# Performance work log

Measured on AMD Instinct MI355X. Metric: run time of the kernel, lower is better.

## Reference

```python
import jax, jax.numpy as jnp
from jax import lax
import numpy as np

H = 512      # hidden_size
NF = 64      # nfeatures
NL = 2       # num_layers
OUT = 1      # output_size
B, T = 64, 512


def _uniform(key, shape, scale):
    return jax.random.uniform(key, shape, jnp.float32, -scale, scale)


def setup_inputs() -> dict:
    key = jax.random.key(0)
    ks = jax.random.split(key, 12)
    s = 1.0 / np.sqrt(H)  # PyTorch LSTM/Linear init scale
    return {
        "x": jax.random.normal(ks[0], (B, T, NF), jnp.float32),
        # layer 0 (input NF -> H), PyTorch gate order i,f,g,o along 4H axis
        "W_ih0": _uniform(ks[1], (4 * H, NF), s),
        "W_hh0": _uniform(ks[2], (4 * H, H), s),
        "b_ih0": _uniform(ks[3], (4 * H,), s),
        "b_hh0": _uniform(ks[4], (4 * H,), s),
        # layer 1 (input H -> H)
        "W_ih1": _uniform(ks[5], (4 * H, H), s),
        "W_hh1": _uniform(ks[6], (4 * H, H), s),
        "b_ih1": _uniform(ks[7], (4 * H,), s),
        "b_hh1": _uniform(ks[8], (4 * H,), s),
        # final linear head
        "W_fc": _uniform(ks[9], (OUT, H), s),
        "b_fc": _uniform(ks[10], (OUT,), s),
    }


def _lstm_layer(x, W_ih, W_hh, b_ih, b_hh):
    """x: [B, T, D_in] -> hidden sequence [B, T, H]. Zero initial state."""
    b, t, _ = x.shape
    h0 = jnp.zeros((b, H), x.dtype)
    c0 = jnp.zeros((b, H), x.dtype)
    # precompute input projections for all timesteps: [T, B, 4H]
    xp = jnp.swapaxes(jnp.einsum('btd,gd->btg', x, W_ih) + b_ih + b_hh, 0, 1)

    def step(carry, xt):
        h, c = carry
        gates = xt + h @ W_hh.T  # [B, 4H]
        i, f, g, o = jnp.split(gates, 4, axis=-1)
        i = jax.nn.sigmoid(i)
        f = jax.nn.sigmoid(f)
        g = jnp.tanh(g)
        o = jax.nn.sigmoid(o)
        c = f * c + i * g
        h = o * jnp.tanh(c)
        return (h, c), h

    _, hs = lax.scan(step, (h0, c0), xp)  # hs: [T, B, H]
    return jnp.swapaxes(hs, 0, 1)


def reference(x, W_ih0, W_hh0, b_ih0, b_hh0, W_ih1, W_hh1, b_ih1, b_hh1, W_fc, b_fc):
    h = _lstm_layer(x, W_ih0, W_hh0, b_ih0, b_hh0)
    h = _lstm_layer(h, W_ih1, W_hh1, b_ih1, b_hh1)
    return h @ W_fc.T + b_fc  # [B, T, OUT]
```

## Files before the change

### kernel.cpp

```cpp
#include <hip/hip_runtime.h>

#define T_STEPS 512
#define BATCH   64
#define HID     512
#define NSLICE  32

typedef __attribute__((ext_vector_type(8))) short short8;
typedef __attribute__((ext_vector_type(4))) float f32x4;

__device__ __forceinline__ unsigned short f2bf(float f){
  unsigned u = __float_as_uint(f);
  u += 0x7FFF + ((u >> 16) & 1);
  return (unsigned short)(u >> 16);
}
__device__ __forceinline__ float bf2f(unsigned short s){
  return __uint_as_float(((unsigned)s) << 16);
}
__device__ __forceinline__ f32x4 mfma16(short8 a, short8 b, f32x4 c){
  return __builtin_amdgcn_mfma_f32_16x16x32_bf16(a, b, c, 0, 0, 0);
}
__device__ __forceinline__ float sigf(float x){
  return 1.0f / (1.0f + exp2f(-1.44269504f * x));
}
__device__ __forceinline__ float tanh_(float x){
  float e = exp2f(2.88539008f * x);
  return 1.0f - 2.0f / (1.0f + e);
}

__device__ __forceinline__ void waitGE(int* p, int target){
  int guard = 0;
  while (__hip_atomic_load(p, __ATOMIC_RELAXED, __HIP_MEMORY_SCOPE_AGENT) < target){
    __builtin_amdgcn_s_sleep(1);
    if (++guard > (1 << 22)) break;
  }
  asm volatile("" ::: "memory");
  __builtin_amdgcn_fence(__ATOMIC_ACQUIRE, "workgroup");
}

__device__ __forceinline__ void signal(int* p){
  __builtin_amdgcn_fence(__ATOMIC_RELEASE, "workgroup");
  asm volatile("" ::: "memory");
  __hip_atomic_fetch_add(p, 1, __ATOMIC_RELAXED, __HIP_MEMORY_SCOPE_AGENT);
}

template<int NKB>
__device__ __forceinline__ void loadB(const unsigned short* __restrict__ Wg, int K, int kstart,
                                      int l15, int l4, short8 B[4][NKB]){
  #pragma unroll
  for (int tt = 0; tt < 4; ++tt)
    #pragma unroll
    for (int kb = 0; kb < NKB; ++kb)
      B[tt][kb] = *(const short8*)(Wg + (long)(tt*16 + l15)*K + kstart + kb*32 + l4*8);
}

template<int NKB>
__device__ __forceinline__ void gemmA(const unsigned short* __restrict__ Ab, long rs,
                                      int l15, int l4, const short8 B[4][NKB], f32x4 acc[4][4]){
  #pragma unroll
  for (int kb = 0; kb < NKB; ++kb){
    short8 a[4];
    #pragma unroll
    for (int m = 0; m < 4; ++m)
      a[m] = *(const short8*)(Ab + (long)(m*16 + l15)*rs + kb*32 + l4*8);
    #pragma unroll
    for (int m = 0; m < 4; ++m)
      #pragma unroll
      for (int tt = 0; tt < 4; ++tt)
        acc[m][tt] = mfma16(B[tt][kb], a[m], acc[m][tt]);
  }
}

__device__ __forceinline__ void reduceWrite(float* red, int w, int l15, int l4, f32x4 acc[4][4]){
  #pragma unroll
  for (int m = 0; m < 4; ++m){
    if (m == w) continue;
    int mi = (m > w) ? m - 1 : m;
    #pragma unroll
    for (int tt = 0; tt < 4; ++tt){
      float* p = red + (w*12 + mi*4 + tt)*320 + l15*20 + l4*4;
      *(f32x4*)p = acc[m][tt];
    }
  }
}
__device__ __forceinline__ void reduceRead(const float* red, int w, int l15, int l4,
                                           f32x4 gf[4], f32x4 acc[4][4]){
  #pragma unroll
  for (int tt = 0; tt < 4; ++tt) gf[tt] = acc[w][tt];
  #pragma unroll
  for (int v = 0; v < 4; ++v){
    if (v == w) continue;
    int mi = (w > v) ? w - 1 : w;
    #pragma unroll
    for (int tt = 0; tt < 4; ++tt){
      const float* p = red + (v*12 + mi*4 + tt)*320 + l15*20 + l4*4;
      gf[tt] += *(const f32x4*)p;
    }
  }
}

__device__ __forceinline__ void gatesStore(f32x4 gf[4], f32x4& cst,
                                           unsigned short* __restrict__ hdst){
  f32x4 hh;
  #pragma unroll
  for (int r = 0; r < 4; ++r){
    float iv = sigf(gf[0][r]), fv = sigf(gf[1][r]);
    float gv = tanh_(gf[2][r]), ov = sigf(gf[3][r]);
    float cv = fv * cst[r] + iv * gv;
    cst[r] = cv;
    hh[r] = ov * tanh_(cv);
  }
  unsigned long long pk = (unsigned long long)f2bf(hh[0])
    | ((unsigned long long)f2bf(hh[1]) << 16)
    | ((unsigned long long)f2bf(hh[2]) << 32)
    | ((unsigned long long)f2bf(hh[3]) << 48);
  __hip_atomic_store((unsigned long long*)hdst, pk, __ATOMIC_RELAXED, __HIP_MEMORY_SCOPE_AGENT);
}

template<int NXB, int NHB>
__device__ void l0_loop(int g, int w, int lane,
                        const unsigned short* __restrict__ Wg,
                        const float* __restrict__ bias0,
                        const unsigned short* __restrict__ xb,
                        unsigned short* __restrict__ h0seq,
                        int* cnt0, float* red, int hk0){
  int l15 = lane & 15, l4 = lane >> 4;
  short8 Bx[4][(NXB > 0) ? NXB : 1];
  if constexpr (NXB > 0) loadB<NXB>(Wg, 576, 0, l15, l4, Bx);
  short8 Bh[4][NHB];
  loadB<NHB>(Wg, 576, 64 + hk0, l15, l4, Bh);
  f32x4 bsv[4];
  #pragma unroll
  for (int tt = 0; tt < 4; ++tt) bsv[tt] = *(const f32x4*)&bias0[(g*4 + tt)*16 + l4*4];
  f32x4 cst = {0.f, 0.f, 0.f, 0.f};
  int b = w*16 + l15, colb = g*16 + l4*4;

  for (int t = 0; t < T_STEPS; ++t){
    if (t) waitGE(&cnt0[t-1], NSLICE);
    f32x4 acc[4][4];
    #pragma unroll
    for (int m = 0; m < 4; ++m)
      #pragma unroll
      for (int tt = 0; tt < 4; ++tt) acc[m][tt] = (f32x4){0.f,0.f,0.f,0.f};
    if constexpr (NXB > 0)
      gemmA<NXB>(xb + (long)t*64, (long)T_STEPS*64, l15, l4, Bx, acc);
    if (t)
      gemmA<NHB>(h0seq + (long)(t-1)*BATCH*HID + hk0, HID, l15, l4, Bh, acc);
    reduceWrite(red, w, l15, l4, acc);
    __syncthreads();
    f32x4 gf[4];
    reduceRead(red, w, l15, l4, gf, acc);
    #pragma unroll
    for (int tt = 0; tt < 4; ++tt) gf[tt] += bsv[tt];
    gatesStore(gf, cst, h0seq + (long)t*BATCH*HID + (long)b*HID + colb);
    __syncthreads();
    if (threadIdx.x == 0) signal(&cnt0[t]);
  }
}

__device__ void l1_loop(int g, int w, int lane,
                        const unsigned short* __restrict__ Wg,
                        const float* __restrict__ bias1,
                        const unsigned short* __restrict__ h0seq,
                        unsigned short* __restrict__ h1seq,
                        int* cnt0, int* cnt1, float* red){
  int l15 = lane & 15, l4 = lane >> 4;
  short8 Bh[4][8];
  loadB<8>(Wg, 1024, w*256, l15, l4, Bh);
  f32x4 bsv[4];
  #pragma unroll
  for (int tt = 0; tt < 4; ++tt) bsv[tt] = *(const f32x4*)&bias1[(g*4 + tt)*16 + l4*4];
  f32x4 cst = {0.f, 0.f, 0.f, 0.f};
  int b = w*16 + l15, colb = g*16 + l4*4;

  for (int t = 0; t < T_STEPS; ++t){
    waitGE(&cnt0[t], NSLICE);
    if (t) waitGE(&cnt1[t-1], NSLICE);
    f32x4 acc[4][4];
    #pragma unroll
    for (int m = 0; m < 4; ++m)
      #pragma unroll
      for (int tt = 0; tt < 4; ++tt) acc[m][tt] = (f32x4){0.f,0.f,0.f,0.f};
    if (w < 2)
      gemmA<8>(h0seq + (long)t*BATCH*HID + w*256, HID, l15, l4, Bh, acc);
    else if (t)
      gemmA<8>(h1seq + (long)(t-1)*BATCH*HID + (w-2)*256, HID, l15, l4, Bh, acc);
    reduceWrite(red, w, l15, l4, acc);
    __syncthreads();
    f32x4 gf[4];
    reduceRead(red, w, l15, l4, gf, acc);
    #pragma unroll
    for (int tt = 0; tt < 4; ++tt) gf[tt] += bsv[tt];
    gatesStore(gf, cst, h1seq + (long)t*BATCH*HID + (long)b*HID + colb);
    __syncthreads();
    if (threadIdx.x == 0) signal(&cnt1[t]);
  }
}

extern "C" __global__ void __launch_bounds__(256, 1)
lstm_persist(const unsigned short* __restrict__ Wpk0,
             const unsigned short* __restrict__ Wpk1,
             const float* __restrict__ bias0, const float* __restrict__ bias1,
             const unsigned short* __restrict__ xb,
             unsigned short* __restrict__ h0seq, unsigned short* __restrict__ h1seq,
             int* cnt0, int* cnt1){
  __shared__ float red[15360];
  int wg = blockIdx.x;
  int role = wg >> 5;
  int g = wg & 31;
  int w = threadIdx.x >> 6;
  int lane = threadIdx.x & 63;

  if (role == 0){
    const unsigned short* Wg = Wpk0 + (long)g*4*16*576;
    switch (w){
      case 0:  l0_loop<2,3>(g, 0, lane, Wg, bias0, xb, h0seq, cnt0, red, 0);   break;
      case 1:  l0_loop<0,5>(g, 1, lane, Wg, bias0, xb, h0seq, cnt0, red, 96);  break;
      case 2:  l0_loop<0,4>(g, 2, lane, Wg, bias0, xb, h0seq, cnt0, red, 256); break;
      default: l0_loop<0,4>(g, 3, lane, Wg, bias0, xb, h0seq, cnt0, red, 384); break;
    }
  } else {
    const unsigned short* Wg = Wpk1 + (long)g*4*16*1024;
    l1_loop(g, w, lane, Wg, bias1, h0seq, h1seq, cnt0, cnt1, red);
  }
}

extern "C" __global__ void prep_kernel(const float* __restrict__ x,
    const float* __restrict__ Wih0, const float* __restrict__ Whh0,
    const float* __restrict__ bih0, const float* __restrict__ bhh0,
    const float* __restrict__ Wih1, const float* __restrict__ Whh1,
    const float* __restrict__ bih1, const float* __restrict__ bhh1,
    unsigned short* __restrict__ Wpk0, unsigned short* __restrict__ Wpk1,
    float* __restrict__ bias0, float* __restrict__ bias1,
    unsigned short* __restrict__ xb, int* __restrict__ syncm){
  long gid = (long)blockIdx.x * blockDim.x + threadIdx.x;
  long gs  = (long)gridDim.x * blockDim.x;
  const long NW0 = 32L*4*16*576;
  const long NW1 = 32L*4*16*1024;
  const long NX  = 64L*512*64;

  for (long i = gid; i < NW0; i += gs){
    int k = (int)(i % 576);
    long q = i / 576;
    int r  = (int)(q & 15);
    long q2 = q >> 4;
    int tt = (int)(q2 & 3);
    int g  = (int)(q2 >> 2);
    int row = tt*512 + g*16 + r;
    float v = (k < 64) ? Wih0[(long)row*64 + k] : Whh0[(long)row*512 + (k - 64)];
    Wpk0[i] = f2bf(v);
  }
  for (long i = gid; i < NW1; i += gs){
    int k = (int)(i & 1023);
    long q = i >> 10;
    int r  = (int)(q & 15);
    long q2 = q >> 4;
    int tt = (int)(q2 & 3);
    int g  = (int)(q2 >> 2);
    int row = tt*512 + g*16 + r;
    float v = (k < 512) ? Wih1[(long)row*512 + k] : Whh1[(long)row*512 + (k - 512)];
    Wpk1[i] = f2bf(v);
  }
  for (long i = gid; i < 2048; i += gs){
    int r = (int)(i & 15);
    int tt = (int)((i >> 4) & 3);
    int g  = (int)(i >> 6);
    int row = tt*512 + g*16 + r;
    bias0[i] = bih0[row] + bhh0[row];
    bias1[i] = bih1[row] + bhh1[row];
  }
  for (long i = gid; i < NX; i += gs) xb[i] = f2bf(x[i]);
  for (long i = gid; i < 1024; i += gs) syncm[i] = 0;
}

extern "C" __global__ void head_kernel(const unsigned short* __restrict__ h1seq,
    const float* __restrict__ wfc, const float* __restrict__ bfc,
    float* __restrict__ out){
  int t = blockIdx.x;
  int tid = threadIdx.x;
  int b = tid >> 2, q = tid & 3;
  const unsigned short* hp = h1seq + ((long)t*BATCH + b)*HID + q*128;
  const float* wp = wfc + q*128;
  float s = 0.f;
  #pragma unroll
  for (int i = 0; i < 16; ++i){
    short8 v = *(const short8*)(hp + i*8);
    #pragma unroll
    for (int e = 0; e < 8; ++e)
      s += bf2f((unsigned short)v[e]) * wp[i*8 + e];
  }
  s += __shfl_xor(s, 1, 64);
  s += __shfl_xor(s, 2, 64);
  if (q == 0) out[(long)b*T_STEPS + t] = s + bfc[0];
}

extern "C" void kernel_launch(void* const* d_in, const int* in_sizes, int n_in,
                              void* d_out, int out_size, void* d_ws, size_t ws_size,
                              hipStream_t stream){
  const float* x    = (const float*)d_in[0];
  const float* Wih0 = (const float*)d_in[1];
  const float* Whh0 = (const float*)d_in[2];
  const float* bih0 = (const float*)d_in[3];
  const float* bhh0 = (const float*)d_in[4];
  const float* Wih1 = (const float*)d_in[5];
  const float* Whh1 = (const float*)d_in[6];
  const float* bih1 = (const float*)d_in[7];
  const float* bhh1 = (const float*)d_in[8];
  const float* wfc  = (const float*)d_in[9];
  const float* bfc  = (const float*)d_in[10];
  float* out = (float*)d_out;

  char* p = (char*)d_ws;
  auto carve = [&](size_t bytes) -> void* {
    void* r = (void*)p;
    p += (bytes + 255) & ~(size_t)255;
    return r;
  };
  unsigned short* Wpk0  = (unsigned short*)carve(32L*4*16*576*2);
  unsigned short* Wpk1  = (unsigned short*)carve(32L*4*16*1024*2);
  float* bias0 = (float*)carve(2048*4);
  float* bias1 = (float*)carve(2048*4);
  unsigned short* xb    = (unsigned short*)carve(64L*512*64*2);
  unsigned short* h0seq = (unsigned short*)carve(512L*64*512*2);
  unsigned short* h1seq = (unsigned short*)carve(512L*64*512*2);
  int* syncm   = (int*)carve(4096);
  int* cnt0 = syncm;
  int* cnt1 = syncm + 512;

  hipLaunchKernelGGL(prep_kernel, dim3(1024), dim3(256), 0, stream,
                     x, Wih0, Whh0, bih0, bhh0, Wih1, Whh1, bih1, bhh1,
                     Wpk0, Wpk1, bias0, bias1, xb, syncm);
  hipLaunchKernelGGL(lstm_persist, dim3(64), dim3(256), 0, stream,
                     Wpk0, Wpk1, bias0, bias1, xb, h0seq, h1seq, cnt0, cnt1);
  hipLaunchKernelGGL(head_kernel, dim3(512), dim3(256), 0, stream,
                     h1seq, wfc, bfc, out);
}
```

Measured before the change: 5.249 ms.

## Replace atomic counter barriers with per-block padded flag slots polled by one wave

```diff
diff --git a/kernel.cpp b/kernel.cpp
--- a/kernel.cpp
+++ b/kernel.cpp
@@ -3,7 +3,6 @@
 #define T_STEPS 512
 #define BATCH   64
 #define HID     512
-#define NSLICE  32
 
 typedef __attribute__((ext_vector_type(8))) short short8;
 typedef __attribute__((ext_vector_type(4))) float f32x4;
@@ -27,20 +26,47 @@
   return 1.0f - 2.0f / (1.0f + e);
 }
 
-__device__ __forceinline__ void waitGE(int* p, int target){
-  int guard = 0;
-  while (__hip_atomic_load(p, __ATOMIC_RELAXED, __HIP_MEMORY_SCOPE_AGENT) < target){
-    __builtin_amdgcn_s_sleep(1);
-    if (++guard > (1 << 22)) break;
-  }
+
+__device__ __forceinline__ void pollL0(const int* flags0, int target){
+  if (threadIdx.x < 64){
+    int lane = threadIdx.x;
+    int guard = 0;
+    for (;;){
+      int v = (lane < 32)
+        ? __hip_atomic_load(&flags0[lane*32], __ATOMIC_RELAXED, __HIP_MEMORY_SCOPE_AGENT)
+        : target;
+      if (__ballot(v >= target) == ~0ull) break;
+      __builtin_amdgcn_s_sleep(1);
+      if (++guard > (1 << 20)) break;
+    }
+  }
+  __builtin_amdgcn_fence(__ATOMIC_ACQUIRE, "workgroup");
   asm volatile("" ::: "memory");
+  __syncthreads();
+}
+
+__device__ __forceinline__ void pollL1(const int* flags0, const int* flags1, int t){
+  if (threadIdx.x < 64){
+    int lane = threadIdx.x;
+    const int* p = (lane < 32) ? &flags0[lane*32] : &flags1[(lane-32)*32];
+    int tgt = (lane < 32) ? t + 1 : t;
+    int guard = 0;
+    for (;;){
+      int v = __hip_atomic_load(p, __ATOMIC_RELAXED, __HIP_MEMORY_SCOPE_AGENT);
+      if (__ballot(v >= tgt) == ~0ull) break;
+      __builtin_amdgcn_s_sleep(1);
+      if (++guard > (1 << 20)) break;
+    }
+  }
   __builtin_amdgcn_fence(__ATOMIC_ACQUIRE, "workgroup");
-}
-
-__device__ __forceinline__ void signal(int* p){
+  asm volatile("" ::: "memory");
+  __syncthreads();
+}
+
+__device__ __forceinline__ void signalSlot(int* slot, int val){
   __builtin_amdgcn_fence(__ATOMIC_RELEASE, "workgroup");
   asm volatile("" ::: "memory");
-  __hip_atomic_fetch_add(p, 1, __ATOMIC_RELAXED, __HIP_MEMORY_SCOPE_AGENT);
+  __hip_atomic_store(slot, val, __ATOMIC_RELAXED, __HIP_MEMORY_SCOPE_AGENT);
 }
 
 template<int NKB>
@@ -122,7 +148,7 @@
                         const float* __restrict__ bias0,
                         const unsigned short* __restrict__ xb,
                         unsigned short* __restrict__ h0seq,
-                        int* cnt0, float* red, int hk0){
+                        int* flags0, float* red, int hk0){
   int l15 = lane & 15, l4 = lane >> 4;
   short8 Bx[4][(NXB > 0) ? NXB : 1];
   if constexpr (NXB > 0) loadB<NXB>(Wg, 576, 0, l15, l4, Bx);
@@ -135,7 +161,6 @@
   int b = w*16 + l15, colb = g*16 + l4*4;
 
   for (int t = 0; t < T_STEPS; ++t){
-    if (t) waitGE(&cnt0[t-1], NSLICE);
     f32x4 acc[4][4];
     #pragma unroll
     for (int m = 0; m < 4; ++m)
@@ -143,6 +168,7 @@
       for (int tt = 0; tt < 4; ++tt) acc[m][tt] = (f32x4){0.f,0.f,0.f,0.f};
     if constexpr (NXB > 0)
       gemmA<NXB>(xb + (long)t*64, (long)T_STEPS*64, l15, l4, Bx, acc);
+    if (t) pollL0(flags0, t);
     if (t)
       gemmA<NHB>(h0seq + (long)(t-1)*BATCH*HID + hk0, HID, l15, l4, Bh, acc);
     reduceWrite(red, w, l15, l4, acc);
@@ -153,7 +179,7 @@
     for (int tt = 0; tt < 4; ++tt) gf[tt] += bsv[tt];
     gatesStore(gf, cst, h0seq + (long)t*BATCH*HID + (long)b*HID + colb);
     __syncthreads();
-    if (threadIdx.x == 0) signal(&cnt0[t]);
+    if (threadIdx.x == 0) signalSlot(&flags0[g*32], t + 1);
   }
 }
 
@@ -162,7 +188,7 @@
                         const float* __restrict__ bias1,
                         const unsigned short* __restrict__ h0seq,
                         unsigned short* __restrict__ h1seq,
-                        int* cnt0, int* cnt1, float* red){
+                        int* flags0, int* flags1, float* red){
   int l15 = lane & 15, l4 = lane >> 4;
   short8 Bh[4][8];
   loadB<8>(Wg, 1024, w*256, l15, l4, Bh);
@@ -173,8 +199,7 @@
   int b = w*16 + l15, colb = g*16 + l4*4;
 
   for (int t = 0; t < T_STEPS; ++t){
-    waitGE(&cnt0[t], NSLICE);
-    if (t) waitGE(&cnt1[t-1], NSLICE);
+    pollL1(flags0, flags1, t);
     f32x4 acc[4][4];
     #pragma unroll
     for (int m = 0; m < 4; ++m)
@@ -192,7 +217,7 @@
     for (int tt = 0; tt < 4; ++tt) gf[tt] += bsv[tt];
     gatesStore(gf, cst, h1seq + (long)t*BATCH*HID + (long)b*HID + colb);
     __syncthreads();
-    if (threadIdx.x == 0) signal(&cnt1[t]);
+    if (threadIdx.x == 0) signalSlot(&flags1[g*32], t + 1);
   }
 }
 
@@ -202,7 +227,7 @@
              const float* __restrict__ bias0, const float* __restrict__ bias1,
              const unsigned short* __restrict__ xb,
              unsigned short* __restrict__ h0seq, unsigned short* __restrict__ h1seq,
-             int* cnt0, int* cnt1){
+             int* flags0, int* flags1){
   __shared__ float red[15360];
   int wg = blockIdx.x;
   int role = wg >> 5;
@@ -213,14 +238,14 @@
   if (role == 0){
     const unsigned short* Wg = Wpk0 + (long)g*4*16*576;
     switch (w){
-      case 0:  l0_loop<2,3>(g, 0, lane, Wg, bias0, xb, h0seq, cnt0, red, 0);   break;
-      case 1:  l0_loop<0,5>(g, 1, lane, Wg, bias0, xb, h0seq, cnt0, red, 96);  break;
-      case 2:  l0_loop<0,4>(g, 2, lane, Wg, bias0, xb, h0seq, cnt0, red, 256); break;
-      default: l0_loop<0,4>(g, 3, lane, Wg, bias0, xb, h0seq, cnt0, red, 384); break;
+      case 0:  l0_loop<2,3>(g, 0, lane, Wg, bias0, xb, h0seq, flags0, red, 0);   break;
+      case 1:  l0_loop<0,5>(g, 1, lane, Wg, bias0, xb, h0seq, flags0, red, 96);  break;
+      case 2:  l0_loop<0,4>(g, 2, lane, Wg, bias0, xb, h0seq, flags0, red, 256); break;
+      default: l0_loop<0,4>(g, 3, lane, Wg, bias0, xb, h0seq, flags0, red, 384); break;
     }
   } else {
     const unsigned short* Wg = Wpk1 + (long)g*4*16*1024;
-    l1_loop(g, w, lane, Wg, bias1, h0seq, h1seq, cnt0, cnt1, red);
+    l1_loop(g, w, lane, Wg, bias1, h0seq, h1seq, flags0, flags1, red);
   }
 }
 
@@ -269,7 +294,7 @@
     bias1[i] = bih1[row] + bhh1[row];
   }
   for (long i = gid; i < NX; i += gs) xb[i] = f2bf(x[i]);
-  for (long i = gid; i < 1024; i += gs) syncm[i] = 0;
+  for (long i = gid; i < 2048; i += gs) syncm[i] = 0;
 }
 
 extern "C" __global__ void head_kernel(const unsigned short* __restrict__ h1seq,
@@ -322,15 +347,15 @@
   unsigned short* xb    = (unsigned short*)carve(64L*512*64*2);
   unsigned short* h0seq = (unsigned short*)carve(512L*64*512*2);
   unsigned short* h1seq = (unsigned short*)carve(512L*64*512*2);
-  int* syncm   = (int*)carve(4096);
-  int* cnt0 = syncm;
-  int* cnt1 = syncm + 512;
+  int* syncm   = (int*)carve(8192);
+  int* flags0 = syncm;
+  int* flags1 = syncm + 1024;
 
   hipLaunchKernelGGL(prep_kernel, dim3(1024), dim3(256), 0, stream,
                      x, Wih0, Whh0, bih0, bhh0, Wih1, Whh1, bih1, bhh1,
                      Wpk0, Wpk1, bias0, bias1, xb, syncm);
   hipLaunchKernelGGL(lstm_persist, dim3(64), dim3(256), 0, stream,
-                     Wpk0, Wpk1, bias0, bias1, xb, h0seq, h1seq, cnt0, cnt1);
+                     Wpk0, Wpk1, bias0, bias1, xb, h0seq, h1seq, flags0, flags1);
   hipLaunchKernelGGL(head_kernel, dim3(512), dim3(256), 0, stream,
                      h1seq, wfc, bfc, out);
 }
```

After: 5.261 ms. Within noise of the previous version (+0.2%).

## Replace counter barriers with sentinel-filled data polling for cross-workgroup sync

Applied to the files above, without the earlier changes.

```diff
diff --git a/kernel.cpp b/kernel.cpp
--- a/kernel.cpp
+++ b/kernel.cpp
@@ -3,7 +3,8 @@
 #define T_STEPS 512
 #define BATCH   64
 #define HID     512
-#define NSLICE  32
+#define SENT32  0x7F807F80u
+#define SENT64  0x7F807F807F807F80ull
 
 typedef __attribute__((ext_vector_type(8))) short short8;
 typedef __attribute__((ext_vector_type(4))) float f32x4;
@@ -27,22 +28,6 @@
   return 1.0f - 2.0f / (1.0f + e);
 }
 
-__device__ __forceinline__ void waitGE(int* p, int target){
-  int guard = 0;
-  while (__hip_atomic_load(p, __ATOMIC_RELAXED, __HIP_MEMORY_SCOPE_AGENT) < target){
-    __builtin_amdgcn_s_sleep(1);
-    if (++guard > (1 << 22)) break;
-  }
-  asm volatile("" ::: "memory");
-  __builtin_amdgcn_fence(__ATOMIC_ACQUIRE, "workgroup");
-}
-
-__device__ __forceinline__ void signal(int* p){
-  __builtin_amdgcn_fence(__ATOMIC_RELEASE, "workgroup");
-  asm volatile("" ::: "memory");
-  __hip_atomic_fetch_add(p, 1, __ATOMIC_RELAXED, __HIP_MEMORY_SCOPE_AGENT);
-}
-
 template<int NKB>
 __device__ __forceinline__ void loadB(const unsigned short* __restrict__ Wg, int K, int kstart,
                                       int l15, int l4, short8 B[4][NKB]){
@@ -54,7 +39,7 @@
 }
 
 template<int NKB>
-__device__ __forceinline__ void gemmA(const unsigned short* __restrict__ Ab, long rs,
+__device__ __forceinline__ void gemmX(const unsigned short* __restrict__ Ab, long rs,
                                       int l15, int l4, const short8 B[4][NKB], f32x4 acc[4][4]){
   #pragma unroll
   for (int kb = 0; kb < NKB; ++kb){
@@ -68,6 +53,58 @@
       for (int tt = 0; tt < 4; ++tt)
         acc[m][tt] = mfma16(B[tt][kb], a[m], acc[m][tt]);
   }
+}
+
+template<int NKB>
+__device__ __forceinline__ void pollLoadA(const unsigned short* __restrict__ Ab, long rs,
+                                          int l15, int l4, short8 a[4][NKB]){
+  unsigned long long v[4][NKB][2];
+  int guard = 0;
+  for (;;){
+    #pragma unroll
+    for (int m = 0; m < 4; ++m){
+      const unsigned long long* pm =
+        (const unsigned long long*)(Ab + (long)(m*16 + l15)*rs + l4*8);
+      #pragma unroll
+      for (int kb = 0; kb < NKB; ++kb){
+        v[m][kb][0] = __hip_atomic_load(pm + kb*8,     __ATOMIC_RELAXED, __HIP_MEMORY_SCOPE_AGENT);
+        v[m][kb][1] = __hip_atomic_load(pm + kb*8 + 1, __ATOMIC_RELAXED, __HIP_MEMORY_SCOPE_AGENT);
+      }
+    }
+    bool ok = true;
+    #pragma unroll
+    for (int m = 0; m < 4; ++m)
+      #pragma unroll
+      for (int kb = 0; kb < NKB; ++kb)
+        #pragma unroll
+        for (int j = 0; j < 2; ++j){
+          unsigned lo = (unsigned)v[m][kb][j];
+          unsigned hi = (unsigned)(v[m][kb][j] >> 32);
+          ok = ok && (lo != SENT32) && (hi != SENT32);
+        }
+    if (ok) break;
+    if (++guard > (1 << 18)) break;
+  }
+  #pragma unroll
+  for (int m = 0; m < 4; ++m)
+    #pragma unroll
+    for (int kb = 0; kb < NKB; ++kb){
+      union { unsigned long long q[2]; short8 s; } u;
+      u.q[0] = v[m][kb][0]; u.q[1] = v[m][kb][1];
+      a[m][kb] = u.s;
+    }
+}
+
+template<int NKB>
+__device__ __forceinline__ void mfmaA(const short8 a[4][NKB], const short8 B[4][NKB],
+                                      f32x4 acc[4][4]){
+  #pragma unroll
+  for (int kb = 0; kb < NKB; ++kb)
+    #pragma unroll
+    for (int m = 0; m < 4; ++m)
+      #pragma unroll
+      for (int tt = 0; tt < 4; ++tt)
+        acc[m][tt] = mfma16(B[tt][kb], a[m][kb], acc[m][tt]);
 }
 
 __device__ __forceinline__ void reduceWrite(float* red, int w, int l15, int l4, f32x4 acc[4][4]){
@@ -122,7 +159,7 @@
                         const float* __restrict__ bias0,
                         const unsigned short* __restrict__ xb,
                         unsigned short* __restrict__ h0seq,
-                        int* cnt0, float* red, int hk0){
+                        float* red, int hk0){
   int l15 = lane & 15, l4 = lane >> 4;
   short8 Bx[4][(NXB > 0) ? NXB : 1];
   if constexpr (NXB > 0) loadB<NXB>(Wg, 576, 0, l15, l4, Bx);
@@ -135,25 +172,26 @@
   int b = w*16 + l15, colb = g*16 + l4*4;
 
   for (int t = 0; t < T_STEPS; ++t){
-    if (t) waitGE(&cnt0[t-1], NSLICE);
     f32x4 acc[4][4];
     #pragma unroll
     for (int m = 0; m < 4; ++m)
       #pragma unroll
       for (int tt = 0; tt < 4; ++tt) acc[m][tt] = (f32x4){0.f,0.f,0.f,0.f};
     if constexpr (NXB > 0)
-      gemmA<NXB>(xb + (long)t*64, (long)T_STEPS*64, l15, l4, Bx, acc);
-    if (t)
-      gemmA<NHB>(h0seq + (long)(t-1)*BATCH*HID + hk0, HID, l15, l4, Bh, acc);
+      gemmX<NXB>(xb + (long)t*64, (long)T_STEPS*64, l15, l4, Bx, acc);
+    if (t){
+      short8 ah[4][NHB];
+      pollLoadA<NHB>(h0seq + (long)(t-1)*BATCH*HID + hk0, HID, l15, l4, ah);
+      mfmaA<NHB>(ah, Bh, acc);
+    }
     reduceWrite(red, w, l15, l4, acc);
     __syncthreads();
     f32x4 gf[4];
     reduceRead(red, w, l15, l4, gf, acc);
+    __syncthreads();
     #pragma unroll
     for (int tt = 0; tt < 4; ++tt) gf[tt] += bsv[tt];
     gatesStore(gf, cst, h0seq + (long)t*BATCH*HID + (long)b*HID + colb);
-    __syncthreads();
-    if (threadIdx.x == 0) signal(&cnt0[t]);
   }
 }
 
@@ -162,10 +200,11 @@
                         const float* __restrict__ bias1,
                         const unsigned short* __restrict__ h0seq,
                         unsigned short* __restrict__ h1seq,
-                        int* cnt0, int* cnt1, float* red){
+                        float* red){
   int l15 = lane & 15, l4 = lane >> 4;
-  short8 Bh[4][8];
-  loadB<8>(Wg, 1024, w*256, l15, l4, Bh);
+  short8 Bh0[4][4], Bh1[4][4];
+  loadB<4>(Wg, 1024, w*256,       l15, l4, Bh0);
+  loadB<4>(Wg, 1024, w*256 + 128, l15, l4, Bh1);
   f32x4 bsv[4];
   #pragma unroll
   for (int tt = 0; tt < 4; ++tt) bsv[tt] = *(const f32x4*)&bias1[(g*4 + tt)*16 + l4*4];
@@ -173,26 +212,36 @@
   int b = w*16 + l15, colb = g*16 + l4*4;
 
   for (int t = 0; t < T_STEPS; ++t){
-    waitGE(&cnt0[t], NSLICE);
-    if (t) waitGE(&cnt1[t-1], NSLICE);
     f32x4 acc[4][4];
     #pragma unroll
     for (int m = 0; m < 4; ++m)
       #pragma unroll
       for (int tt = 0; tt < 4; ++tt) acc[m][tt] = (f32x4){0.f,0.f,0.f,0.f};
-    if (w < 2)
-      gemmA<8>(h0seq + (long)t*BATCH*HID + w*256, HID, l15, l4, Bh, acc);
-    else if (t)
-      gemmA<8>(h1seq + (long)(t-1)*BATCH*HID + (w-2)*256, HID, l15, l4, Bh, acc);
+    if (w < 2){
+      const unsigned short* src = h0seq + (long)t*BATCH*HID + w*256;
+      short8 a0[4][4];
+      pollLoadA<4>(src, HID, l15, l4, a0);
+      mfmaA<4>(a0, Bh0, acc);
+      short8 a1[4][4];
+      pollLoadA<4>(src + 128, HID, l15, l4, a1);
+      mfmaA<4>(a1, Bh1, acc);
+    } else if (t){
+      const unsigned short* src = h1seq + (long)(t-1)*BATCH*HID + (w-2)*256;
+      short8 a0[4][4];
+      pollLoadA<4>(src, HID, l15, l4, a0);
+      mfmaA<4>(a0, Bh0, acc);
+      short8 a1[4][4];
+      pollLoadA<4>(src + 128, HID, l15, l4, a1);
+      mfmaA<4>(a1, Bh1, acc);
+    }
     reduceWrite(red, w, l15, l4, acc);
     __syncthreads();
     f32x4 gf[4];
     reduceRead(red, w, l15, l4, gf, acc);
+    __syncthreads();
     #pragma unroll
     for (int tt = 0; tt < 4; ++tt) gf[tt] += bsv[tt];
     gatesStore(gf, cst, h1seq + (long)t*BATCH*HID + (long)b*HID + colb);
-    __syncthreads();
-    if (threadIdx.x == 0) signal(&cnt1[t]);
   }
 }
 
@@ -201,8 +250,7 @@
              const unsigned short* __restrict__ Wpk1,
              const float* __restrict__ bias0, const float* __restrict__ bias1,
              const unsigned short* __restrict__ xb,
-             unsigned short* __restrict__ h0seq, unsigned short* __restrict__ h1seq,
-             int* cnt0, int* cnt1){
+             unsigned short* __restrict__ h0seq, unsigned short* __restrict__ h1seq){
   __shared__ float red[15360];
   int wg = blockIdx.x;
   int role = wg >> 5;
@@ -213,14 +261,14 @@
   if (role == 0){
     const unsigned short* Wg = Wpk0 + (long)g*4*16*576;
     switch (w){
-      case 0:  l0_loop<2,3>(g, 0, lane, Wg, bias0, xb, h0seq, cnt0, red, 0);   break;
-      case 1:  l0_loop<0,5>(g, 1, lane, Wg, bias0, xb, h0seq, cnt0, red, 96);  break;
-      case 2:  l0_loop<0,4>(g, 2, lane, Wg, bias0, xb, h0seq, cnt0, red, 256); break;
-      default: l0_loop<0,4>(g, 3, lane, Wg, bias0, xb, h0seq, cnt0, red, 384); break;
+      case 0:  l0_loop<2,3>(g, 0, lane, Wg, bias0, xb, h0seq, red, 0);   break;
+      case 1:  l0_loop<0,5>(g, 1, lane, Wg, bias0, xb, h0seq, red, 96);  break;
+      case 2:  l0_loop<0,4>(g, 2, lane, Wg, bias0, xb, h0seq, red, 256); break;
+      default: l0_loop<0,4>(g, 3, lane, Wg, bias0, xb, h0seq, red, 384); break;
     }
   } else {
     const unsigned short* Wg = Wpk1 + (long)g*4*16*1024;
-    l1_loop(g, w, lane, Wg, bias1, h0seq, h1seq, cnt0, cnt1, red);
+    l1_loop(g, w, lane, Wg, bias1, h0seq, h1seq, red);
   }
 }
 
@@ -231,12 +279,14 @@
     const float* __restrict__ bih1, const float* __restrict__ bhh1,
     unsigned short* __restrict__ Wpk0, unsigned short* __restrict__ Wpk1,
     float* __restrict__ bias0, float* __restrict__ bias1,
-    unsigned short* __restrict__ xb, int* __restrict__ syncm){
+    unsigned short* __restrict__ xb,
+    unsigned long long* __restrict__ h0p, unsigned long long* __restrict__ h1p){
   long gid = (long)blockIdx.x * blockDim.x + threadIdx.x;
   long gs  = (long)gridDim.x * blockDim.x;
   const long NW0 = 32L*4*16*576;
   const long NW1 = 32L*4*16*1024;
   const long NX  = 64L*512*64;
+  const long NH8 = (long)T_STEPS*BATCH*HID/4;
 
   for (long i = gid; i < NW0; i += gs){
     int k = (int)(i % 576);
@@ -269,7 +319,7 @@
     bias1[i] = bih1[row] + bhh1[row];
   }
   for (long i = gid; i < NX; i += gs) xb[i] = f2bf(x[i]);
-  for (long i = gid; i < 1024; i += gs) syncm[i] = 0;
+  for (long i = gid; i < NH8; i += gs){ h0p[i] = SENT64; h1p[i] = SENT64; }
 }
 
 extern "C" __global__ void head_kernel(const unsigned short* __restrict__ h1seq,
@@ -322,15 +372,13 @@
   unsigned short* xb    = (unsigned short*)carve(64L*512*64*2);
   unsigned short* h0seq = (unsigned short*)carve(512L*64*512*2);
   unsigned short* h1seq = (unsigned short*)carve(512L*64*512*2);
-  int* syncm   = (int*)carve(4096);
-  int* cnt0 = syncm;
-  int* cnt1 = syncm + 512;
 
   hipLaunchKernelGGL(prep_kernel, dim3(1024), dim3(256), 0, stream,
                      x, Wih0, Whh0, bih0, bhh0, Wih1, Whh1, bih1, bhh1,
-                     Wpk0, Wpk1, bias0, bias1, xb, syncm);
+                     Wpk0, Wpk1, bias0, bias1, xb,
+                     (unsigned long long*)h0seq, (unsigned long long*)h1seq);
   hipLaunchKernelGGL(lstm_persist, dim3(64), dim3(256), 0, stream,
-                     Wpk0, Wpk1, bias0, bias1, xb, h0seq, h1seq, cnt0, cnt1);
+                     Wpk0, Wpk1, bias0, bias1, xb, h0seq, h1seq);
   hipLaunchKernelGGL(head_kernel, dim3(512), dim3(256), 0, stream,
                      h1seq, wfc, bfc, out);
 }
```

New measurement: 6.644 ms. 26.6% more time.
